# Optimization experiments

Hardware: AMD Instinct MI355X
Metric: run time of the kernel (lower is better)

The kernel has to match this reference:

```python
import jax, jax.numpy as jnp
import numpy as np

B, S, T, H, VS, VT = 64, 64, 64, 1024, 32000, 32000


def _init(key, shape, scale=0.05):
    return scale * jax.random.normal(key, shape, dtype=jnp.float32)


def setup_inputs() -> dict:
    key = jax.random.key(0)
    ks = jax.random.split(key, 16)
    source = jax.random.randint(ks[0], (B, S), 0, VS)
    target = jax.random.randint(ks[1], (B, T), 0, VT)
    emb_src = _init(ks[2], (VS, H)).at[0].set(0.0)   # padding_idx=0
    emb_tgt = _init(ks[3], (VT, H)).at[0].set(0.0)   # padding_idx=0
    W_ih_enc = _init(ks[4], (4 * H, H)); W_hh_enc = _init(ks[5], (4 * H, H))
    b_ih_enc = _init(ks[6], (4 * H,));   b_hh_enc = _init(ks[7], (4 * H,))
    W_ih_dec = _init(ks[8], (4 * H, H)); W_hh_dec = _init(ks[9], (4 * H, H))
    b_ih_dec = _init(ks[10], (4 * H,));  b_hh_dec = _init(ks[11], (4 * H,))
    W_att = _init(ks[12], (H, 2 * H));   b_att = _init(ks[13], (H,))
    W_out = _init(ks[14], (VT, H));      b_out = _init(ks[15], (VT,))
    return dict(source=source, target=target, emb_src=emb_src, emb_tgt=emb_tgt,
                W_ih_enc=W_ih_enc, W_hh_enc=W_hh_enc, b_ih_enc=b_ih_enc, b_hh_enc=b_hh_enc,
                W_ih_dec=W_ih_dec, W_hh_dec=W_hh_dec, b_ih_dec=b_ih_dec, b_hh_dec=b_hh_dec,
                W_att=W_att, b_att=b_att, W_out=W_out, b_out=b_out)


def _lstm_cell(x, h, c, W_ih, W_hh, b):
    # PyTorch gate order: i, f, g, o
    gates = x @ W_ih.T + h @ W_hh.T + b
    i, f, g, o = jnp.split(gates, 4, axis=-1)
    c_new = jax.nn.sigmoid(f) * c + jax.nn.sigmoid(i) * jnp.tanh(g)
    h_new = jax.nn.sigmoid(o) * jnp.tanh(c_new)
    return h_new, c_new


def reference(source, target, emb_src, emb_tgt,
              W_ih_enc, W_hh_enc, b_ih_enc, b_hh_enc,
              W_ih_dec, W_hh_dec, b_ih_dec, b_hh_dec,
              W_att, b_att, W_out, b_out):
    src = source.T              # [S, B]
    tgt = target.T              # [T, B]
    h0 = jnp.zeros((B, H), jnp.float32)
    c0 = jnp.zeros((B, H), jnp.float32)

    # ---- Encoder: time-major LSTM via scan (dropout in eval mode = identity) ----
    x_src = emb_src[src]        # [S, B, H]
    b_enc = b_ih_enc + b_hh_enc

    def enc_step(carry, x_t):
        h, c = carry
        h, c = _lstm_cell(x_t, h, c, W_ih_enc, W_hh_enc, b_enc)
        return (h, c), h

    (hT, cT), hx_list = jax.lax.scan(enc_step, (h0, c0), x_src)  # hx_list: [S, B, H]

    # ---- Decoder: hx_cx is never updated in the original loop, so every
    # timestep uses the SAME encoder final state -> fully vectorizable over t ----
    words_f = tgt[: S - 1]      # [Td, B], Td = T-1 (S == T)
    words_t = tgt[1:]           # [Td, B]
    x_dec = emb_tgt[words_f]    # [Td, B, H]
    b_dec = b_ih_dec + b_hh_dec
    gates = x_dec @ W_ih_dec.T + (hT @ W_hh_dec.T + b_dec)[None]  # [Td, B, 4H]
    i, f, g, o = jnp.split(gates, 4, axis=-1)
    c_new = jax.nn.sigmoid(f) * cT[None] + jax.nn.sigmoid(i) * jnp.tanh(g)
    hx = jax.nn.sigmoid(o) * jnp.tanh(c_new)                       # [Td, B, H]

    # ---- Attention (dot-product over source positions, softmax over S) ----
    scores = jnp.einsum('tbh,sbh->tsb', hx, hx_list)               # [Td, S, B]
    neg_inf = jnp.asarray(-jnp.inf, jnp.float32)
    mask = (src != 0)[None]                                        # [1, S, B]
    scores = jnp.where(mask, scores, neg_inf)
    align = jax.nn.softmax(scores, axis=1)                         # over S
    content = jnp.einsum('tsb,sbh->tbh', align, hx_list)           # [Td, B, H]
    concat = jnp.concatenate([content, hx], axis=-1)               # [Td, B, 2H]
    hx_att = jnp.tanh(concat @ W_att.T + b_att)                    # [Td, B, H]

    # ---- Output projection + per-step cross entropy (ignore_index=0), summed ----
    logits = hx_att @ W_out.T + b_out                              # [Td, B, VT]
    logp = jax.nn.log_softmax(logits, axis=-1)
    nll = -jnp.take_along_axis(logp, words_t[..., None], axis=-1).squeeze(-1)  # [Td, B]
    valid = (words_t != 0).astype(jnp.float32)
    per_step = jnp.sum(nll * valid, axis=1) / jnp.maximum(jnp.sum(valid, axis=1), 1.0)
    return jnp.sum(per_step)
```

## Files before the change

### kernel.cpp

```cpp
#include <hip/hip_runtime.h>
#include <math.h>

#define Bb 64
#define Ss 64
#define Hh 1024
#define Vv 32000
#define RD 4032
#define RP 4096
#define NT4 4096
#define ENC_NBLK 64

typedef unsigned short u16;
typedef unsigned long long u64;
typedef __attribute__((ext_vector_type(8))) short bf16x8;
typedef __attribute__((ext_vector_type(4))) float f32x4;

#define MFMA(a, b, c) __builtin_amdgcn_mfma_f32_16x16x32_bf16(a, b, c, 0, 0, 0)

__device__ __forceinline__ u16 f2b(float f) {
  union { float f; unsigned u; } v; v.f = f;
  unsigned r = v.u + 0x7fffu + ((v.u >> 16) & 1u);
  return (u16)(r >> 16);
}
__device__ __forceinline__ float b2f(u16 b) {
  union { unsigned u; float f; } v; v.u = ((unsigned)b) << 16; return v.f;
}
__device__ __forceinline__ float sigf(float x) { return 1.f / (1.f + expf(-x)); }

__device__ __forceinline__ u64 AL(const u64* p) {
  return __hip_atomic_load(p, __ATOMIC_RELAXED, __HIP_MEMORY_SCOPE_AGENT);
}
__device__ __forceinline__ void AS(u64* p, u64 v) {
  __hip_atomic_store(p, v, __ATOMIC_RELAXED, __HIP_MEMORY_SCOPE_AGENT);
}
__device__ __forceinline__ int AL32(const int* p) {
  return __hip_atomic_load(p, __ATOMIC_RELAXED, __HIP_MEMORY_SCOPE_AGENT);
}
__device__ __forceinline__ void AS32(int* p, int v) {
  __hip_atomic_store(p, v, __ATOMIC_RELAXED, __HIP_MEMORY_SCOPE_AGENT);
}

__device__ __forceinline__ void gll16(const void* g, void* l) {
  __builtin_amdgcn_global_load_lds(
      (const __attribute__((address_space(1))) unsigned int*)g,
      (__attribute__((address_space(3))) unsigned int*)l, 16, 0, 0);
}

__global__ void k_fail(float* out) { out[0] = 1e30f; }

__global__ void k_cvt_all(const float* __restrict__ s0, u16* __restrict__ d0,
                          const float* __restrict__ s1, u16* __restrict__ d1,
                          const float* __restrict__ s2, u16* __restrict__ d2,
                          const float* __restrict__ s3, u16* __restrict__ d3,
                          const float* __restrict__ s4, u16* __restrict__ d4,
                          const float* __restrict__ s5, u16* __restrict__ d5) {
  const int A4 = NT4 * Hh / 4;
  const int E4 = Hh * 2048 / 4;
  const int F4 = Vv * Hh / 4;
  const int TOT = 4 * A4 + E4 + F4;
  const int st = gridDim.x * blockDim.x;
  for (int i = blockIdx.x * blockDim.x + threadIdx.x; i < TOT; i += st) {
    const float* sp; u16* dp; int off;
    if (i < A4)            { sp = s0; dp = d0; off = i; }
    else if (i < 2 * A4)   { sp = s1; dp = d1; off = i - A4; }
    else if (i < 3 * A4)   { sp = s2; dp = d2; off = i - 2 * A4; }
    else if (i < 4 * A4)   { sp = s3; dp = d3; off = i - 3 * A4; }
    else if (i < 4 * A4 + E4) { sp = s4; dp = d4; off = i - 4 * A4; }
    else                   { sp = s5; dp = d5; off = i - 4 * A4 - E4; }
    const float4 v = ((const float4*)sp)[off];
    ushort4 o; o.x = f2b(v.x); o.y = f2b(v.y); o.z = f2b(v.z); o.w = f2b(v.w);
    ((ushort4*)dp)[off] = o;
  }
}

__global__ void k_gather2(const int* __restrict__ src_tok, const float* __restrict__ emb_s,
                          u16* __restrict__ out_s,
                          const int* __restrict__ tgt_tok, const float* __restrict__ emb_t,
                          u16* __restrict__ out_t) {
  int r = blockIdx.x;
  const int* tok; const float* emb; u16* outp; int nstep;
  if (r < RP) { tok = src_tok; emb = emb_s; outp = out_s; nstep = 64; }
  else        { r -= RP; tok = tgt_tok; emb = emb_t; outp = out_t; nstep = 63; }
  const int step = r >> 6, b = r & 63;
  const int idx = (step < nstep) ? tok[b * 64 + step] : 0;
  const float4 v = ((const float4*)(emb + (size_t)idx * Hh))[threadIdx.x];
  ushort4 o; o.x = f2b(v.x); o.y = f2b(v.y); o.z = f2b(v.z); o.w = f2b(v.w);
  ((ushort4*)(outp + (size_t)r * Hh))[threadIdx.x] = o;
}

__device__ __forceinline__ void dg_tile(const u16* __restrict__ A, const u16* __restrict__ Bm,
                                        u16* __restrict__ C, int bx, int by,
                                        u16* As, u16* Bs) {
  const int tid = threadIdx.x;
  const int wave = tid >> 6, lane = tid & 63;
  const int l15 = lane & 15, lhi = lane >> 4;
  const int m0 = by * 128, n0 = bx * 128;
  const int wm = (wave >> 1) * 64, wn = (wave & 1) * 64;
  f32x4 acc[4][4] = {};
  const int srow = wave * 32 + (lane >> 3);
  const int scolb = (lane & 7) * 16;
  for (int k0 = 0; k0 < Hh; k0 += 64) {
    __syncthreads();
#pragma unroll
    for (int q = 0; q < 4; ++q) {
      const int r = srow + q * 8;
      gll16((const char*)(A + (size_t)(m0 + r) * Hh + k0) + scolb,
            (char*)As + (wave * 32 + q * 8) * 128);
      gll16((const char*)(Bm + (size_t)(n0 + r) * Hh + k0) + scolb,
            (char*)Bs + (wave * 32 + q * 8) * 128);
    }
    __syncthreads();
#pragma unroll
    for (int kk = 0; kk < 2; ++kk) {
      const int ko = kk * 32 + lhi * 8;
      bf16x8 af[4], bfr[4];
#pragma unroll
      for (int i = 0; i < 4; ++i) af[i] = *(const bf16x8*)(As + (wm + i * 16 + l15) * 64 + ko);
#pragma unroll
      for (int j = 0; j < 4; ++j) bfr[j] = *(const bf16x8*)(Bs + (wn + j * 16 + l15) * 64 + ko);
#pragma unroll
      for (int i = 0; i < 4; ++i)
#pragma unroll
        for (int j = 0; j < 4; ++j)
          acc[i][j] = MFMA(af[i], bfr[j], acc[i][j]);
    }
  }
#pragma unroll
  for (int i = 0; i < 4; ++i) {
    const int gr = m0 + wm + i * 16 + lhi * 4;
#pragma unroll
    for (int j = 0; j < 4; ++j) {
      const int gc = n0 + wn + j * 16 + l15;
#pragma unroll
      for (int rr = 0; rr < 4; ++rr)
        C[(size_t)(gr + rr) * NT4 + gc] = f2b(acc[i][j][rr]);
    }
  }
}

__global__ __launch_bounds__(256)
void k_pre2(const u16* __restrict__ Ae, const u16* __restrict__ Be, u16* __restrict__ Ce,
            const u16* __restrict__ Ad, const u16* __restrict__ Bd, u16* __restrict__ Cd) {
  __shared__ __align__(16) u16 As[128 * 64];
  __shared__ __align__(16) u16 Bs[128 * 64];
  int t = blockIdx.x;
  if (t < 1024) dg_tile(Ae, Be, Ce, t & 31, t >> 5, As, Bs);
  else { t -= 1024; dg_tile(Ad, Bd, Cd, t & 31, t >> 5, As, Bs); }
}

template<int EPI>
__global__ __launch_bounds__(256)
void k_gemm(const u16* __restrict__ A, const u16* __restrict__ Bm,
            void* __restrict__ C, int M, int N, int K,
            const float* __restrict__ bias,
            float* __restrict__ pmax, float* __restrict__ psum, int ncols) {
  __shared__ __align__(16) u16 As[128 * 64];
  __shared__ __align__(16) u16 Bs[128 * 64];
  const int tid = threadIdx.x;
  const int wave = tid >> 6, lane = tid & 63;
  const int l15 = lane & 15, lhi = lane >> 4;
  int bx = blockIdx.x, by = blockIdx.y;
  {
    const int gx_ = gridDim.x, gy_ = gridDim.y;
    const int nwg = gx_ * gy_;
    if ((gy_ & 3) == 0 && (gx_ & 1) == 0) {
      const int f = by * gx_ + bx;
      const int x = f & 7, i = f >> 3;
      const int rby = gy_ >> 2, hx = gx_ >> 1;
      by = (x >> 1) * rby + (i % rby);
      bx = (x & 1) * hx + (i / rby);
    } else if ((nwg & 7) == 0) {
      int flat = by * gx_ + bx;
      const int qq = nwg >> 3;
      flat = (flat & 7) * qq + (flat >> 3);
      bx = flat % gx_; by = flat / gx_;
    }
  }
  const int m0 = by * 128, n0 = bx * 128;
  const int wm = (wave >> 1) * 64, wn = (wave & 1) * 64;
  f32x4 acc[4][4] = {};
  const int srow = wave * 32 + (lane >> 3);
  const int scolb = (lane & 7) * 16;

  for (int k0 = 0; k0 < K; k0 += 64) {
    __syncthreads();
#pragma unroll
    for (int q = 0; q < 4; ++q) {
      const int r = srow + q * 8;
      int ra = m0 + r; ra = (ra < M) ? ra : (M - 1);
      gll16((const char*)(A + (size_t)ra * K + k0) + scolb,
            (char*)As + (wave * 32 + q * 8) * 128);
      gll16((const char*)(Bm + (size_t)(n0 + r) * K + k0) + scolb,
            (char*)Bs + (wave * 32 + q * 8) * 128);
    }
    __syncthreads();
#pragma unroll
    for (int kk = 0; kk < 2; ++kk) {
      const int ko = kk * 32 + lhi * 8;
      bf16x8 af[4], bfr[4];
#pragma unroll
      for (int i = 0; i < 4; ++i) af[i] = *(const bf16x8*)(As + (wm + i * 16 + l15) * 64 + ko);
#pragma unroll
      for (int j = 0; j < 4; ++j) bfr[j] = *(const bf16x8*)(Bs + (wn + j * 16 + l15) * 64 + ko);
#pragma unroll
      for (int i = 0; i < 4; ++i)
#pragma unroll
        for (int j = 0; j < 4; ++j)
          acc[i][j] = MFMA(af[i], bfr[j], acc[i][j]);
    }
  }

  if (EPI == 0) {
#pragma unroll
    for (int i = 0; i < 4; ++i) {
      const int gr = m0 + wm + i * 16 + lhi * 4;
#pragma unroll
      for (int j = 0; j < 4; ++j) {
        const int gc = n0 + wn + j * 16 + l15;
        const float bv = bias ? bias[gc] : 0.f;
#pragma unroll
        for (int rr = 0; rr < 4; ++rr)
          ((float*)C)[(size_t)(gr + rr) * N + gc] = acc[i][j][rr] + bv;
      }
    }
  } else if (EPI == 3) {
#pragma unroll
    for (int i = 0; i < 4; ++i) {
      const int gr = m0 + wm + i * 16 + lhi * 4;
#pragma unroll
      for (int j = 0; j < 4; ++j) {
        const int gc = n0 + wn + j * 16 + l15;
        const float bv = bias[gc];
#pragma unroll
        for (int rr = 0; rr < 4; ++rr)
          ((u16*)C)[(size_t)(gr + rr) * N + gc] = f2b(tanhf(acc[i][j][rr] + bv));
      }
    }
  } else {
    float bj[4];
#pragma unroll
    for (int j = 0; j < 4; ++j) bj[j] = bias[n0 + wn + j * 16 + l15];
    const int pc = bx * 2 + (wn ? 1 : 0);
#pragma unroll
    for (int i = 0; i < 4; ++i) {
#pragma unroll
      for (int rr = 0; rr < 4; ++rr) {
        float v0 = acc[i][0][rr] + bj[0];
        float v1 = acc[i][1][rr] + bj[1];
        float v2 = acc[i][2][rr] + bj[2];
        float v3 = acc[i][3][rr] + bj[3];
        float m = fmaxf(fmaxf(v0, v1), fmaxf(v2, v3));
#pragma unroll
        for (int d = 1; d < 16; d <<= 1) m = fmaxf(m, __shfl_xor(m, d, 64));
        float s = __expf(v0 - m) + __expf(v1 - m) + __expf(v2 - m) + __expf(v3 - m);
#pragma unroll
        for (int d = 1; d < 16; d <<= 1) s += __shfl_xor(s, d, 64);
        if (l15 == 0) {
          const int grow = m0 + wm + i * 16 + lhi * 4 + rr;
          pmax[(size_t)grow * ncols + pc] = m;
          psum[(size_t)grow * ncols + pc] = s;
        }
      }
    }
  }
}

__global__ __launch_bounds__(256, 1)
void k_enc_all(const u16* __restrict__ Wb, const u16* __restrict__ gx,
               const float* __restrict__ b_ih, const float* __restrict__ b_hh,
               u16* __restrict__ hxl, float* __restrict__ c_out, int* flags) {
  __shared__ __align__(16) u16 Ws[64 * 1024];
  __shared__ float Gs[64 * 65];
  __shared__ float bsum[64];
  const int tid = threadIdx.x;
  const int wave = tid >> 6, lane = tid & 63;
  const int l15 = lane & 15, lhi = lane >> 4;
  const int c0 = blockIdx.x * 16;
  const int cb = tid >> 2, cq = tid & 3;
  const int rot = blockIdx.x & 31;

  for (int i = tid; i < 64 * 128; i += 256) {
    const int r = i >> 7, ck = i & 127;
    const int grow = (r >> 4) * Hh + c0 + (r & 15);
    const int bo = (ck * 16) ^ ((r & 7) << 4);
    *(bf16x8*)((char*)Ws + r * 2048 + bo) = *(const bf16x8*)(Wb + (size_t)grow * Hh + ck * 8);
  }
  if (tid < 64) {
    const int col = (tid >> 4) * Hh + c0 + (tid & 15);
    bsum[tid] = b_ih[col] + b_hh[col];
  }
  float creg[4] = {0.f, 0.f, 0.f, 0.f};
  __syncthreads();

  for (int s = 0; s < 64; ++s) {
    u64 graw[4];
#pragma unroll
    for (int g = 0; g < 4; ++g)
      graw[g] = *(const u64*)(gx + (size_t)(s * 64 + cb) * NT4 + g * Hh + c0 + cq * 4);

    f32x4 acc[4] = {};
    if (s > 0) {
      if (wave == 0) {
        for (;;) {
          const int f = AL32(flags + blockIdx.x * 64 + lane);
          if (__all(f >= s)) break;
          __builtin_amdgcn_s_sleep(1);
        }
      }
      __syncthreads();
      const u64* apw = (const u64*)(hxl + ((size_t)(s - 1) * 64 + wave * 16 + l15) * Hh);
      const char* wsb = (const char*)Ws;
      const int xr = (l15 & 7) << 4;
#pragma unroll 8
      for (int i = 0; i < 32; ++i) {
        const int kf = (i + rot) & 31;
        const int k = kf * 32 + lhi * 8;
        const u64 ua = AL(apw + (k >> 2));
        const u64 ub = AL(apw + (k >> 2) + 1);
        union { u64 qq[2]; bf16x8 v; } cv;
        cv.qq[0] = ua; cv.qq[1] = ub;
        const int kb = (k * 2) ^ xr;
#pragma unroll
        for (int nt = 0; nt < 4; ++nt)
          acc[nt] = MFMA(cv.v, *(const bf16x8*)(wsb + (nt * 16 + l15) * 2048 + kb), acc[nt]);
      }
    }
#pragma unroll
    for (int nt = 0; nt < 4; ++nt)
#pragma unroll
      for (int r = 0; r < 4; ++r)
        Gs[(wave * 16 + lhi * 4 + r) * 65 + nt * 16 + l15] = acc[nt][r];
    __syncthreads();
    {
      const float* gsrow = Gs + cb * 65;
      u64 pk = 0;
#pragma unroll
      for (int j = 0; j < 4; ++j) {
        const int col = cq * 4 + j;
        const float gi = gsrow[col]      + b2f((u16)(graw[0] >> (16 * j))) + bsum[col];
        const float gf = gsrow[16 + col] + b2f((u16)(graw[1] >> (16 * j))) + bsum[16 + col];
        const float gg = gsrow[32 + col] + b2f((u16)(graw[2] >> (16 * j))) + bsum[32 + col];
        const float go = gsrow[48 + col] + b2f((u16)(graw[3] >> (16 * j))) + bsum[48 + col];
        const float cn = sigf(gf) * creg[j] + sigf(gi) * tanhf(gg);
        const float hv = sigf(go) * tanhf(cn);
        creg[j] = cn;
        pk |= (u64)f2b(hv) << (16 * j);
      }
      AS((u64*)(hxl + ((size_t)s * 64 + cb) * Hh + c0 + cq * 4), pk);
    }
    __syncthreads();
    if (tid < ENC_NBLK)
      AS32(flags + tid * 64 + blockIdx.x, s + 1);
  }
#pragma unroll
  for (int j = 0; j < 4; ++j)
    c_out[cb * Hh + c0 + cq * 4 + j] = creg[j];
}

__global__ void k_dec_cell(const u16* __restrict__ G, const float* __restrict__ dbase,
                           const float* __restrict__ cT, const float* __restrict__ b_ih,
                           const float* __restrict__ b_hh, u16* __restrict__ Acat) {
  const int idx = blockIdx.x * 256 + threadIdx.x;
  const int r = idx >> 8, c4 = (idx & 255) * 4;
  if (r >= RD) return;
  const int b = r & 63;
  u64 graw[4]; f32x4 dv[4], bi[4], bh[4];
#pragma unroll
  for (int g = 0; g < 4; ++g) {
    graw[g] = *(const u64*)(G + (size_t)r * NT4 + g * Hh + c4);
    dv[g] = *(const f32x4*)(dbase + (size_t)b * NT4 + g * Hh + c4);
    bi[g] = *(const f32x4*)(b_ih + g * Hh + c4);
    bh[g] = *(const f32x4*)(b_hh + g * Hh + c4);
  }
  const f32x4 cv4 = *(const f32x4*)(cT + b * Hh + c4);
  u64 pk = 0;
#pragma unroll
  for (int j = 0; j < 4; ++j) {
    const float gi = b2f((u16)(graw[0] >> (16 * j))) + dv[0][j] + bi[0][j] + bh[0][j];
    const float gf = b2f((u16)(graw[1] >> (16 * j))) + dv[1][j] + bi[1][j] + bh[1][j];
    const float gg = b2f((u16)(graw[2] >> (16 * j))) + dv[2][j] + bi[2][j] + bh[2][j];
    const float go = b2f((u16)(graw[3] >> (16 * j))) + dv[3][j] + bi[3][j] + bh[3][j];
    const float cn = sigf(gf) * cv4[j] + sigf(gi) * tanhf(gg);
    const float hv = sigf(go) * tanhf(cn);
    pk |= (u64)f2b(hv) << (16 * j);
  }
  *(u64*)(Acat + (size_t)r * 2048 + Hh + c4) = pk;
}

__global__ __launch_bounds__(256)
void k_attn_b(u16* __restrict__ Acat, const u16* __restrict__ hxl,
              const int* __restrict__ src) {
  __shared__ __align__(16) u16 hs[64 * 1024];
  __shared__ float qs[1024];
  __shared__ float prob[64];
  __shared__ int mflag[64];
  const int b = blockIdx.x >> 2, th = blockIdx.x & 3;
  const int tid = threadIdx.x, wave = tid >> 6, lane = tid & 63;
#pragma unroll 8
  for (int i = 0; i < 32; ++i) {
    const int c = i * 4 + wave;
    gll16((const char*)(hxl + ((size_t)(c >> 1) * 64 + b) * Hh + (c & 1) * 512) + lane * 16,
          (char*)hs + c * 1024 + lane * 16);
  }
  if (tid < 64) mflag[tid] = (src[b * 64 + tid] != 0);
  __syncthreads();
  const int t0 = th * 16;
  const int tEnd = (t0 + 16 < 63) ? t0 + 16 : 63;
  for (int t = t0; t < tEnd; ++t) {
    const size_t r = (size_t)t * 64 + b;
    {
      const u64 q4 = *(const u64*)(Acat + r * 2048 + Hh + tid * 4);
      qs[tid * 4 + 0] = b2f((u16)q4);
      qs[tid * 4 + 1] = b2f((u16)(q4 >> 16));
      qs[tid * 4 + 2] = b2f((u16)(q4 >> 32));
      qs[tid * 4 + 3] = b2f((u16)(q4 >> 48));
    }
    __syncthreads();
    for (int sub = 0; sub < 16; ++sub) {
      const int ss = wave * 16 + sub;
      float p = 0.f;
#pragma unroll
      for (int q = 0; q < 4; ++q) {
        const int i4 = lane + 64 * q;
        const ushort4 v = *(const ushort4*)(hs + ss * 1024 + i4 * 4);
        p += qs[i4 * 4 + 0] * b2f(v.x) + qs[i4 * 4 + 1] * b2f(v.y)
           + qs[i4 * 4 + 2] * b2f(v.z) + qs[i4 * 4 + 3] * b2f(v.w);
      }
#pragma unroll
      for (int d = 1; d < 64; d <<= 1) p += __shfl_xor(p, d, 64);
      if (lane == 0) prob[ss] = mflag[ss] ? p : -INFINITY;
    }
    __syncthreads();
    if (wave == 0) {
      const float v = prob[lane];
      float m = v;
#pragma unroll
      for (int d = 1; d < 64; d <<= 1) m = fmaxf(m, __shfl_xor(m, d, 64));
      const float e = __expf(v - m);
      float ssum = e;
#pragma unroll
      for (int d = 1; d < 64; d <<= 1) ssum += __shfl_xor(ssum, d, 64);
      prob[lane] = e / ssum;
    }
    __syncthreads();
    float4 a4 = {0.f, 0.f, 0.f, 0.f};
    for (int s2 = 0; s2 < 64; ++s2) {
      const float a = prob[s2];
      const ushort4 v = *(const ushort4*)(hs + s2 * 1024 + tid * 4);
      a4.x += a * b2f(v.x); a4.y += a * b2f(v.y);
      a4.z += a * b2f(v.z); a4.w += a * b2f(v.w);
    }
    const u64 pk = (u64)f2b(a4.x) | ((u64)f2b(a4.y) << 16)
                 | ((u64)f2b(a4.z) << 32) | ((u64)f2b(a4.w) << 48);
    *(u64*)(Acat + r * 2048 + tid * 4) = pk;
    __syncthreads();
  }
}

__global__ void k_lsetl(const float* __restrict__ pmax, const float* __restrict__ psum,
                        const u16* __restrict__ hx_att_b, const int* __restrict__ target,
                        const float* __restrict__ W, const float* __restrict__ bo,
                        float* __restrict__ nll, int ncols) {
  const int r = blockIdx.x * 4 + (threadIdx.x >> 6);
  const int lane = threadIdx.x & 63;
  if (r >= RD) return;
  float m = -INFINITY;
  for (int i = lane; i < ncols; i += 64) m = fmaxf(m, pmax[(size_t)r * ncols + i]);
#pragma unroll
  for (int d = 1; d < 64; d <<= 1) m = fmaxf(m, __shfl_xor(m, d, 64));
  float s = 0.f;
  for (int i = lane; i < ncols; i += 64)
    s += psum[(size_t)r * ncols + i] * __expf(pmax[(size_t)r * ncols + i] - m);
#pragma unroll
  for (int d = 1; d < 64; d <<= 1) s += __shfl_xor(s, d, 64);
  const int t = r >> 6, b = r & 63;
  const int w = target[b * 64 + t + 1];
  const u16* a = hx_att_b + (size_t)r * Hh;
  const float* wr = W + (size_t)w * Hh;
  float p = 0.f;
  for (int h = lane; h < Hh; h += 64) p += b2f(a[h]) * wr[h];
#pragma unroll
  for (int d = 1; d < 64; d <<= 1) p += __shfl_xor(p, d, 64);
  if (lane == 0) nll[r] = (m + logf(s)) - (p + bo[w]);
}

__global__ void k_final(const float* __restrict__ nll, const int* __restrict__ target,
                        float* __restrict__ out) {
  const int t = threadIdx.x;
  float ps = 0.f;
  if (t < 63) {
    float sn = 0.f, cnt = 0.f;
    for (int b = 0; b < 64; ++b) {
      const int r = t * 64 + b;
      const int w = target[b * 64 + t + 1];
      if (w != 0) { sn += nll[r]; cnt += 1.f; }
    }
    ps = sn / fmaxf(cnt, 1.f);
  }
#pragma unroll
  for (int d = 1; d < 64; d <<= 1) ps += __shfl_xor(ps, d, 64);
  if (t == 0) out[0] = ps;
}

extern "C" void kernel_launch(void* const* d_in, const int* in_sizes, int n_in,
                              void* d_out, int out_size, void* d_ws, size_t ws_size,
                              hipStream_t stream) {
  const int*   source   = (const int*)d_in[0];
  const int*   target   = (const int*)d_in[1];
  const float* emb_src  = (const float*)d_in[2];
  const float* emb_tgt  = (const float*)d_in[3];
  const float* W_ih_enc = (const float*)d_in[4];
  const float* W_hh_enc = (const float*)d_in[5];
  const float* b_ih_enc = (const float*)d_in[6];
  const float* b_hh_enc = (const float*)d_in[7];
  const float* W_ih_dec = (const float*)d_in[8];
  const float* W_hh_dec = (const float*)d_in[9];
  const float* b_ih_dec = (const float*)d_in[10];
  const float* b_hh_dec = (const float*)d_in[11];
  const float* W_att    = (const float*)d_in[12];
  const float* b_att    = (const float*)d_in[13];
  const float* W_out    = (const float*)d_in[14];
  const float* b_out    = (const float*)d_in[15];
  float* out = (float*)d_out;

  char* base = (char*)d_ws;
  size_t off = 0;
  auto alloc = [&](size_t bytes) -> void* {
    void* r = base + off; off += (bytes + 255) & ~(size_t)255; return r;
  };
  u16*   wb_ih_enc = (u16*)alloc((size_t)NT4 * Hh * 2);
  u16*   wb_hh_enc = (u16*)alloc((size_t)NT4 * Hh * 2);
  u16*   wb_ih_dec = (u16*)alloc((size_t)NT4 * Hh * 2);
  u16*   wb_hh_dec = (u16*)alloc((size_t)NT4 * Hh * 2);
  u16*   wb_att    = (u16*)alloc((size_t)Hh * 2048 * 2);
  u16*   wb_out    = (u16*)alloc((size_t)Vv * Hh * 2);
  u16*   x_src_b   = (u16*)alloc((size_t)RP * Hh * 2);
  u16*   x_dec_b   = (u16*)alloc((size_t)RP * Hh * 2);
  u16*   gates16   = (u16*)alloc((size_t)RP * NT4 * 2);
  u16*   gates_dec = (u16*)alloc((size_t)RP * NT4 * 2);
  u16*   hxl       = (u16*)alloc((size_t)Ss * Bb * Hh * 2);
  float* c_enc     = (float*)alloc((size_t)Bb * Hh * 4);
  float* dbase     = (float*)alloc((size_t)128 * NT4 * 4);
  u16*   Acat      = (u16*)alloc((size_t)RP * 2048 * 2);
  u16*   hx_att_b  = (u16*)alloc((size_t)RP * Hh * 2);
  float* pmax      = (float*)alloc((size_t)RP * 500 * 4);
  float* psum      = (float*)alloc((size_t)RP * 500 * 4);
  float* nll       = (float*)alloc((size_t)RD * 4);
  int*   flags     = (int*)alloc(ENC_NBLK * ENC_NBLK * 4);

  if (off > ws_size) { k_fail<<<1, 1, 0, stream>>>(out); return; }

  k_cvt_all<<<2048, 256, 0, stream>>>(W_ih_enc, wb_ih_enc, W_hh_enc, wb_hh_enc,
                                      W_ih_dec, wb_ih_dec, W_hh_dec, wb_hh_dec,
                                      W_att, wb_att, W_out, wb_out);

  hipMemsetAsync(flags, 0, ENC_NBLK * ENC_NBLK * 4, stream);

  k_gather2<<<2 * RP, 256, 0, stream>>>(source, emb_src, x_src_b,
                                        target, emb_tgt, x_dec_b);

  k_pre2<<<2048, 256, 0, stream>>>(x_src_b, wb_ih_enc, gates16,
                                   x_dec_b, wb_ih_dec, gates_dec);

  k_enc_all<<<ENC_NBLK, 256, 0, stream>>>(wb_hh_enc, gates16, b_ih_enc, b_hh_enc,
                                          hxl, c_enc, flags);

  k_gemm<0><<<dim3(32, 1), 256, 0, stream>>>(hxl + (size_t)63 * Bb * Hh, wb_hh_dec, dbase,
                                             64, NT4, Hh, nullptr, nullptr, nullptr, 0);
  k_dec_cell<<<RD, 256, 0, stream>>>(gates_dec, dbase, c_enc, b_ih_dec, b_hh_dec, Acat);

  k_attn_b<<<256, 256, 0, stream>>>(Acat, hxl, source);

  k_gemm<3><<<dim3(8, 32), 256, 0, stream>>>(Acat, wb_att, hx_att_b, RP, Hh, 2048,
                                             b_att, nullptr, nullptr, 0);

  k_gemm<2><<<dim3(250, 32), 256, 0, stream>>>(hx_att_b, wb_out, nullptr, RP, Vv, Hh,
                                               b_out, pmax, psum, 500);
  k_lsetl<<<(RD + 3) / 4, 256, 0, stream>>>(pmax, psum, hx_att_b, target, W_out, b_out,
                                            nll, 500);
  k_final<<<1, 64, 0, stream>>>(nll, target, out);
}
```

Before: 1.571 ms.

## Replace encoder flag barrier with sentinel-polled data-ready hidden state loads

The encoder's cross-block synchronisation via per-step flag arrays is replaced by filling the hidden-state buffer with an all-ones sentinel and having each wave poll its own needed hidden words until none equal the sentinel. Hidden values are speculatively loaded into registers right after each step and only missing words are reloaded. This removes the flag write, flag poll and one block barrier per step, at the cost of 64 extra u64 registers per thread and a full memset of the hidden buffer. It relies on no valid bf16x4 packed value equalling the sentinel (all-NaN pattern), and on 64-bit stores being atomic.

```diff
diff --git a/kernel.cpp b/kernel.cpp
--- a/kernel.cpp
+++ b/kernel.cpp
@@ -9,6 +9,7 @@
 #define RP 4096
 #define NT4 4096
 #define ENC_NBLK 64
+#define SENT 0xFFFFFFFFFFFFFFFFULL
 
 typedef unsigned short u16;
 typedef unsigned long long u64;
@@ -31,12 +32,6 @@
   return __hip_atomic_load(p, __ATOMIC_RELAXED, __HIP_MEMORY_SCOPE_AGENT);
 }
 __device__ __forceinline__ void AS(u64* p, u64 v) {
-  __hip_atomic_store(p, v, __ATOMIC_RELAXED, __HIP_MEMORY_SCOPE_AGENT);
-}
-__device__ __forceinline__ int AL32(const int* p) {
-  return __hip_atomic_load(p, __ATOMIC_RELAXED, __HIP_MEMORY_SCOPE_AGENT);
-}
-__device__ __forceinline__ void AS32(int* p, int v) {
   __hip_atomic_store(p, v, __ATOMIC_RELAXED, __HIP_MEMORY_SCOPE_AGENT);
 }
 
@@ -268,7 +263,7 @@
 __global__ __launch_bounds__(256, 1)
 void k_enc_all(const u16* __restrict__ Wb, const u16* __restrict__ gx,
                const float* __restrict__ b_ih, const float* __restrict__ b_hh,
-               u16* __restrict__ hxl, float* __restrict__ c_out, int* flags) {
+               u16* __restrict__ hxl, float* __restrict__ c_out) {
   __shared__ __align__(16) u16 Ws[64 * 1024];
   __shared__ float Gs[64 * 65];
   __shared__ float bsum[64];
@@ -292,6 +287,7 @@
   float creg[4] = {0.f, 0.f, 0.f, 0.f};
   __syncthreads();
 
+  u64 ha[32], hb[32];
   for (int s = 0; s < 64; ++s) {
     u64 graw[4];
 #pragma unroll
@@ -300,26 +296,27 @@
 
     f32x4 acc[4] = {};
     if (s > 0) {
-      if (wave == 0) {
-        for (;;) {
-          const int f = AL32(flags + blockIdx.x * 64 + lane);
-          if (__all(f >= s)) break;
-          __builtin_amdgcn_s_sleep(1);
+      const u64* apw = (const u64*)(hxl + ((size_t)(s - 1) * 64 + wave * 16 + l15) * Hh);
+      for (;;) {
+        bool miss = false;
+#pragma unroll
+        for (int i = 0; i < 32; ++i) {
+          const int kw = ((i + rot) & 31) * 8 + lhi * 2;
+          if (ha[i] == SENT) ha[i] = AL(apw + kw);
+          if (hb[i] == SENT) hb[i] = AL(apw + kw + 1);
+          miss |= (ha[i] == SENT) | (hb[i] == SENT);
         }
-      }
-      __syncthreads();
-      const u64* apw = (const u64*)(hxl + ((size_t)(s - 1) * 64 + wave * 16 + l15) * Hh);
+        if (!__any(miss)) break;
+        __builtin_amdgcn_s_sleep(1);
+      }
       const char* wsb = (const char*)Ws;
       const int xr = (l15 & 7) << 4;
-#pragma unroll 8
+#pragma unroll
       for (int i = 0; i < 32; ++i) {
         const int kf = (i + rot) & 31;
-        const int k = kf * 32 + lhi * 8;
-        const u64 ua = AL(apw + (k >> 2));
-        const u64 ub = AL(apw + (k >> 2) + 1);
         union { u64 qq[2]; bf16x8 v; } cv;
-        cv.qq[0] = ua; cv.qq[1] = ub;
-        const int kb = (k * 2) ^ xr;
+        cv.qq[0] = ha[i]; cv.qq[1] = hb[i];
+        const int kb = ((kf * 32 + lhi * 8) * 2) ^ xr;
 #pragma unroll
         for (int nt = 0; nt < 4; ++nt)
           acc[nt] = MFMA(cv.v, *(const bf16x8*)(wsb + (nt * 16 + l15) * 2048 + kb), acc[nt]);
@@ -348,9 +345,16 @@
       }
       AS((u64*)(hxl + ((size_t)s * 64 + cb) * Hh + c0 + cq * 4), pk);
     }
-    __syncthreads();
-    if (tid < ENC_NBLK)
-      AS32(flags + tid * 64 + blockIdx.x, s + 1);
+    if (s < 63) {
+      const u64* apn = (const u64*)(hxl + ((size_t)s * 64 + wave * 16 + l15) * Hh);
+#pragma unroll
+      for (int i = 0; i < 32; ++i) {
+        const int kw = ((i + rot) & 31) * 8 + lhi * 2;
+        ha[i] = AL(apn + kw);
+        hb[i] = AL(apn + kw + 1);
+      }
+    }
+    __syncthreads();
   }
 #pragma unroll
   for (int j = 0; j < 4; ++j)
@@ -546,7 +550,6 @@
   float* pmax      = (float*)alloc((size_t)RP * 500 * 4);
   float* psum      = (float*)alloc((size_t)RP * 500 * 4);
   float* nll       = (float*)alloc((size_t)RD * 4);
-  int*   flags     = (int*)alloc(ENC_NBLK * ENC_NBLK * 4);
 
   if (off > ws_size) { k_fail<<<1, 1, 0, stream>>>(out); return; }
 
@@ -554,7 +557,7 @@
                                       W_ih_dec, wb_ih_dec, W_hh_dec, wb_hh_dec,
                                       W_att, wb_att, W_out, wb_out);
 
-  hipMemsetAsync(flags, 0, ENC_NBLK * ENC_NBLK * 4, stream);
+  hipMemsetAsync(hxl, 0xFF, (size_t)Ss * Bb * Hh * 2, stream);
 
   k_gather2<<<2 * RP, 256, 0, stream>>>(source, emb_src, x_src_b,
                                         target, emb_tgt, x_dec_b);
@@ -563,7 +566,7 @@
                                    x_dec_b, wb_ih_dec, gates_dec);
 
   k_enc_all<<<ENC_NBLK, 256, 0, stream>>>(wb_hh_enc, gates16, b_ih_enc, b_hh_enc,
-                                          hxl, c_enc, flags);
+                                          hxl, c_enc);
 
   k_gemm<0><<<dim3(32, 1), 256, 0, stream>>>(hxl + (size_t)63 * Bb * Hh, wb_hh_dec, dbase,
                                              64, NT4, Hh, nullptr, nullptr, nullptr, 0);
```

Measured after the change: 1.832 ms. 1.17x slower.

## Replace LDS-staged batched attention with one block per decoder row

Applied to the files above, without the earlier changes.

The attention kernel used to launch 256 blocks, each staging a batch's full encoder history (128 KB) in shared memory and looping over 16 decoder steps. It now launches one block per decoder row (4032 blocks) and reads the encoder states straight from global memory or cache. This drops the large LDS footprint, which capped occupancy at one block per CU and left the GPU underfilled. The cost is that each row re-reads the 128 KB history, adding global and L2 traffic.

```diff
diff --git a/kernel.cpp b/kernel.cpp
--- a/kernel.cpp
+++ b/kernel.cpp
@@ -388,73 +388,51 @@
 }
 
 __global__ __launch_bounds__(256)
-void k_attn_b(u16* __restrict__ Acat, const u16* __restrict__ hxl,
-              const int* __restrict__ src) {
-  __shared__ __align__(16) u16 hs[64 * 1024];
-  __shared__ float qs[1024];
-  __shared__ float prob[64];
-  __shared__ int mflag[64];
-  const int b = blockIdx.x >> 2, th = blockIdx.x & 3;
+void k_attn(u16* Acat, const u16* __restrict__ hxl, const int* __restrict__ src) {
+  __shared__ float qs[Hh];
+  __shared__ float sc[Ss];
+  const int r = blockIdx.x;
+  const int b = r & 63;
   const int tid = threadIdx.x, wave = tid >> 6, lane = tid & 63;
-#pragma unroll 8
-  for (int i = 0; i < 32; ++i) {
-    const int c = i * 4 + wave;
-    gll16((const char*)(hxl + ((size_t)(c >> 1) * 64 + b) * Hh + (c & 1) * 512) + lane * 16,
-          (char*)hs + c * 1024 + lane * 16);
-  }
-  if (tid < 64) mflag[tid] = (src[b * 64 + tid] != 0);
+  for (int h = tid; h < Hh; h += 256) qs[h] = b2f(Acat[(size_t)r * 2048 + Hh + h]);
   __syncthreads();
-  const int t0 = th * 16;
-  const int tEnd = (t0 + 16 < 63) ? t0 + 16 : 63;
-  for (int t = t0; t < tEnd; ++t) {
-    const size_t r = (size_t)t * 64 + b;
-    {
-      const u64 q4 = *(const u64*)(Acat + r * 2048 + Hh + tid * 4);
-      qs[tid * 4 + 0] = b2f((u16)q4);
-      qs[tid * 4 + 1] = b2f((u16)(q4 >> 16));
-      qs[tid * 4 + 2] = b2f((u16)(q4 >> 32));
-      qs[tid * 4 + 3] = b2f((u16)(q4 >> 48));
-    }
-    __syncthreads();
-    for (int sub = 0; sub < 16; ++sub) {
-      const int ss = wave * 16 + sub;
-      float p = 0.f;
-#pragma unroll
-      for (int q = 0; q < 4; ++q) {
-        const int i4 = lane + 64 * q;
-        const ushort4 v = *(const ushort4*)(hs + ss * 1024 + i4 * 4);
-        p += qs[i4 * 4 + 0] * b2f(v.x) + qs[i4 * 4 + 1] * b2f(v.y)
-           + qs[i4 * 4 + 2] * b2f(v.z) + qs[i4 * 4 + 3] * b2f(v.w);
-      }
-#pragma unroll
-      for (int d = 1; d < 64; d <<= 1) p += __shfl_xor(p, d, 64);
-      if (lane == 0) prob[ss] = mflag[ss] ? p : -INFINITY;
-    }
-    __syncthreads();
-    if (wave == 0) {
-      const float v = prob[lane];
-      float m = v;
-#pragma unroll
-      for (int d = 1; d < 64; d <<= 1) m = fmaxf(m, __shfl_xor(m, d, 64));
-      const float e = __expf(v - m);
-      float ssum = e;
-#pragma unroll
-      for (int d = 1; d < 64; d <<= 1) ssum += __shfl_xor(ssum, d, 64);
-      prob[lane] = e / ssum;
-    }
-    __syncthreads();
-    float4 a4 = {0.f, 0.f, 0.f, 0.f};
-    for (int s2 = 0; s2 < 64; ++s2) {
-      const float a = prob[s2];
-      const ushort4 v = *(const ushort4*)(hs + s2 * 1024 + tid * 4);
-      a4.x += a * b2f(v.x); a4.y += a * b2f(v.y);
-      a4.z += a * b2f(v.z); a4.w += a * b2f(v.w);
-    }
-    const u64 pk = (u64)f2b(a4.x) | ((u64)f2b(a4.y) << 16)
-                 | ((u64)f2b(a4.z) << 32) | ((u64)f2b(a4.w) << 48);
-    *(u64*)(Acat + r * 2048 + tid * 4) = pk;
-    __syncthreads();
-  }
+  for (int sub = 0; sub < 16; ++sub) {
+    const int ss = wave * 16 + sub;
+    const ushort4* hp4 = (const ushort4*)(hxl + ((size_t)ss * Bb + b) * Hh);
+    float p = 0.f;
+#pragma unroll
+    for (int q = 0; q < 4; ++q) {
+      const int i4 = lane + 64 * q;
+      const ushort4 v = hp4[i4];
+      p += qs[i4 * 4 + 0] * b2f(v.x) + qs[i4 * 4 + 1] * b2f(v.y)
+         + qs[i4 * 4 + 2] * b2f(v.z) + qs[i4 * 4 + 3] * b2f(v.w);
+    }
+#pragma unroll
+    for (int d = 1; d < 64; d <<= 1) p += __shfl_xor(p, d, 64);
+    if (lane == 0) sc[ss] = (src[b * 64 + ss] != 0) ? p : -INFINITY;
+  }
+  __syncthreads();
+  if (wave == 0) {
+    const float v = sc[lane];
+    float m = v;
+#pragma unroll
+    for (int d = 1; d < 64; d <<= 1) m = fmaxf(m, __shfl_xor(m, d, 64));
+    const float e = __expf(v - m);
+    float ssum = e;
+#pragma unroll
+    for (int d = 1; d < 64; d <<= 1) ssum += __shfl_xor(ssum, d, 64);
+    sc[lane] = e / ssum;
+  }
+  __syncthreads();
+  float4 a4 = {0.f, 0.f, 0.f, 0.f};
+  for (int s2 = 0; s2 < 64; ++s2) {
+    const float a = sc[s2];
+    const ushort4 v = *(const ushort4*)(hxl + ((size_t)s2 * Bb + b) * Hh + tid * 4);
+    a4.x += a * b2f(v.x); a4.y += a * b2f(v.y);
+    a4.z += a * b2f(v.z); a4.w += a * b2f(v.w);
+  }
+  u16* dst = Acat + (size_t)r * 2048 + tid * 4;
+  dst[0] = f2b(a4.x); dst[1] = f2b(a4.y); dst[2] = f2b(a4.z); dst[3] = f2b(a4.w);
 }
 
 __global__ void k_lsetl(const float* __restrict__ pmax, const float* __restrict__ psum,
@@ -569,7 +547,7 @@
                                              64, NT4, Hh, nullptr, nullptr, nullptr, 0);
   k_dec_cell<<<RD, 256, 0, stream>>>(gates_dec, dbase, c_enc, b_ih_dec, b_hh_dec, Acat);
 
-  k_attn_b<<<256, 256, 0, stream>>>(Acat, hxl, source);
+  k_attn<<<RD, 256, 0, stream>>>(Acat, hxl, source);
 
   k_gemm<3><<<dim3(8, 32), 256, 0, stream>>>(Acat, wb_att, hx_att_b, RP, Hh, 2048,
                                              b_att, nullptr, nullptr, 0);
```

Result: faster. 1.506 ms (-4.1%).
